# Kernel tuning notes

Measured on AMD Instinct MI355X. Metric: run time of the kernel, lower is better.

## Reference

```python
import jax, jax.numpy as jnp
import numpy as np

EPS = 1e-5      # BatchNorm eps
QLEV = 255.0    # 8-bit PACT activation levels (unsigned)
WMAX = 127.0    # int8 symmetric weight range


def _ste(x, q):
    # straight-through estimator: forward value q, gradient of x
    return x + jax.lax.stop_gradient(q - x)


def _wquant(w):
    # channel-wise symmetric int8 fake-quant of conv weights (per out-channel)
    s = jnp.maximum(jnp.max(jnp.abs(w), axis=(1, 2, 3), keepdims=True) / WMAX, 1e-8)
    q = jnp.clip(jnp.round(w / s), -WMAX, WMAX) * s
    return _ste(w, q)


def _conv3x3(x, w, stride=1):
    return jax.lax.conv_general_dilated(
        x, w, window_strides=(stride, stride), padding=((1, 1), (1, 1)),
        dimension_numbers=("NCHW", "OIHW", "NCHW"))


def _bn(x, g, b, m, v):
    # folded BatchNorm: per-channel affine with running stats
    return (x - m) * (g * jax.lax.rsqrt(v + EPS)) + b


def _pact(x, alpha):
    # PACT: clip to [0, alpha] then 8-bit per-channel fake-quant
    c = jnp.clip(x, 0.0, alpha)
    s = alpha / QLEV
    q = jnp.round(c / s) * s
    return _ste(c, q)


def _requant(x, s):
    # requantize onto common grid s (shift-based align in the int model)
    return _ste(x, jnp.round(x / s) * s)


def setup_inputs() -> dict:
    key = jax.random.key(0)
    ks = jax.random.split(key, 10)
    N, C, H, W = 32, 128, 56, 56
    x = jax.random.normal(ks[0], (N, C, H, W), jnp.float32)
    w1 = jax.random.normal(ks[1], (C, C, 3, 3), jnp.float32) * 0.05
    w2 = jax.random.normal(ks[2], (C, C, 3, 3), jnp.float32) * 0.05
    pc = (1, C, 1, 1)
    g1 = jnp.ones(pc, jnp.float32); b1 = jnp.zeros(pc, jnp.float32)
    m1 = jax.random.normal(ks[3], pc, jnp.float32) * 0.1
    v1 = jax.random.uniform(ks[4], pc, jnp.float32) + 0.5
    g2 = jnp.ones(pc, jnp.float32); b2 = jnp.zeros(pc, jnp.float32)
    m2 = jax.random.normal(ks[5], pc, jnp.float32) * 0.1
    v2 = jax.random.uniform(ks[6], pc, jnp.float32) + 0.5
    a1 = jax.random.uniform(ks[7], pc, jnp.float32) * 2.0 + 2.0
    a2 = jax.random.uniform(ks[8], pc, jnp.float32) * 2.0 + 2.0
    a3 = jax.random.uniform(ks[9], pc, jnp.float32) * 2.0 + 2.0
    return {"x": x, "w1": w1, "g1": g1, "b1": b1, "m1": m1, "v1": v1, "a1": a1,
            "w2": w2, "g2": g2, "b2": b2, "m2": m2, "v2": v2, "a2": a2, "a3": a3}


def reference(x, w1, g1, b1, m1, v1, a1, w2, g2, b2, m2, v2, a2, a3):
    # branch: quant-conv -> BN -> PACT-quant, twice
    out = _pact(_bn(_conv3x3(x, _wquant(w1)), g1, b1, m1, v1), a1)
    out = _pact(_bn(_conv3x3(out, _wquant(w2)), g2, b2, m2, v2), a2)
    # shift-based residual add: align both operands to act3's quant grid, add, clip+quant
    s3 = a3 / QLEV
    y = _requant(out, s3) + _requant(x, s3)
    return _pact(y, a3)
```

## Files before the change

kernel.cpp:

```cpp
#include <hip/hip_runtime.h>
#include <cstdint>

typedef __attribute__((ext_vector_type(4))) float f32x4;
typedef __attribute__((ext_vector_type(2))) float f32x2;
typedef __attribute__((ext_vector_type(4))) int int4v;
typedef __attribute__((ext_vector_type(4))) uint32_t uint4v;

#define EPSV 1e-5f

#define IMG   3136
#define NPIX  100352
#define PADTOT 13778944
#define S1Q (8.0f/127.0f)
#define S2Q (8.0f/(127.0f*254.0f))
#define S1A (4.0f/127.0f)
#define S2A (4.0f/(127.0f*254.0f))

#define UNPX 384
#define UNB  49152

__global__ __launch_bounds__(256) void k_prep(
    const float* __restrict__ x, const float* __restrict__ w1, const float* __restrict__ w2,
    const float* __restrict__ g1, const float* __restrict__ b1, const float* __restrict__ m1,
    const float* __restrict__ v1, const float* __restrict__ a1,
    const float* __restrict__ g2, const float* __restrict__ b2, const float* __restrict__ m2,
    const float* __restrict__ v2, const float* __restrict__ a2, const float* __restrict__ a3,
    int8_t* __restrict__ xq1, int8_t* __restrict__ xq2,
    int8_t* __restrict__ wj1, int8_t* __restrict__ wj2,
    char* __restrict__ o1k1, char* __restrict__ o1k2,
    f32x4* __restrict__ pp1, f32x4* __restrict__ pp2, f32x4* __restrict__ pp3,
    short* __restrict__ j3, int use_j3) {
  __shared__ float shf[7296];
  const int bid = blockIdx.x;
  const int t = threadIdx.x;

  if (bid < 1792) {
    int n = bid / 56, h = bid - (bid / 56) * 56;
    const float* base = x + (size_t)n * 401408 + h * 56;
    for (int idx = t; idx < 7168; idx += 256) {
      int ci = idx / 56, w = idx - (idx / 56) * 56;
      shf[ci * 57 + w] = base[ci * 3136 + w];
    }
    __syncthreads();
    const int ob = ((n * 58 + h + 1) * 58 + 1) * 128;
    for (int idx = t; idx < 1792; idx += 256) {
      int w = idx >> 5, c4 = (idx & 31) * 4;
      uint32_t p1 = 0, p2 = 0;
#pragma unroll
      for (int j = 0; j < 4; ++j) {
        float v = shf[(c4 + j) * 57 + w];
        float j1 = rintf(v * (127.0f / 8.0f));
        j1 = fminf(fmaxf(j1, -127.f), 127.f);
        float rr = v - j1 * S1Q;
        float j2 = rintf(rr * ((127.0f * 254.0f) / 8.0f));
        j2 = fminf(fmaxf(j2, -127.f), 127.f);
        p1 |= ((uint32_t)((int)j1 & 0xff)) << (8 * j);
        p2 |= ((uint32_t)((int)j2 & 0xff)) << (8 * j);
      }
      *(uint32_t*)(xq1 + ob + w * 128 + c4) = p1;
      *(uint32_t*)(xq2 + ob + w * 128 + c4) = p2;
    }
    if (use_j3) {
      const size_t jb = (size_t)n * 401408 + h * 56;
      for (int idx = t; idx < 7168; idx += 256) {
        int ci = idx / 56, w = idx - (idx / 56) * 56;
        float inv3 = 255.0f / a3[ci];
        j3[jb + ci * 3136 + w] = (short)(int)rintf(shf[ci * 57 + w] * inv3);
      }
    }
  } else if (bid < 1792 + 912) {
    int i = (bid - 1792) * 256 + t;
    int bi = i / 58368;
    int j = i - bi * 58368;
    char* buf = (bi == 0) ? (char*)xq1 : (bi == 1) ? (char*)xq2 : (bi == 2) ? o1k1 : o1k2;
    int n = j / 1824, cid = j - n * 1824;
    const int rowc = 58 * 8;
    int chunk;
    if (cid < rowc) chunk = cid;
    else if (cid < 2 * rowc) chunk = 57 * rowc + (cid - rowc);
    else {
      int e = cid - 2 * rowc;
      int h = 1 + (e >> 4);
      int r = e & 15;
      int w = (r < 8) ? 0 : 57;
      chunk = h * rowc + w * 8 + (r & 7);
    }
    long addr = ((long)n * 26912 + chunk) * 16;
    *(uint4v*)(buf + addr) = (uint4v){0u, 0u, 0u, 0u};
  } else {
    int sub = bid - 2704;
    int o = sub & 127;
    bool second = sub >= 128;
    const float* src = (second ? w2 : w1) + o * 1152;
    int8_t* wj = second ? wj2 : wj1;
    float* red = shf;
    float m = 0.f;
    for (int i = t; i < 1152; i += 256) m = fmaxf(m, fabsf(src[i]));
    red[t] = m;
    __syncthreads();
    for (int s = 128; s > 0; s >>= 1) {
      if (t < s) red[t] = fmaxf(red[t], red[t + s]);
      __syncthreads();
    }
    float s = fmaxf(red[0] / 127.0f, 1e-8f);
    for (int i = t; i < 1152; i += 256) {
      float q = rintf(src[i] / s);
      q = fminf(fmaxf(q, -127.f), 127.f);
      int ci = i / 9, tap = i - ci * 9;
      wj[(tap * 128 + o) * 128 + ci] = (int8_t)(int)q;
    }
    if (t == 0) {
      if (!second) {
        float r1 = 1.0f / sqrtf(v1[o] + EPSV);
        float sc1 = g1[o] * r1;
        pp1[o] = (f32x4){s * sc1, b1[o] - m1[o] * sc1, 255.0f / a1[o], a1[o] / 255.0f};
        pp3[o] = (f32x4){a3[o] / 255.0f, 255.0f / a3[o], a3[o], 0.0f};
      } else {
        float r2 = 1.0f / sqrtf(v2[o] + EPSV);
        float sc2 = g2[o] * r2;
        pp2[o] = (f32x4){s * sc2, b2[o] - m2[o] * sc2, 255.0f / a2[o], a2[o] / 255.0f};
      }
    }
  }
}


__global__ __launch_bounds__(512, 2) void k_conv1(
    const int8_t* __restrict__ xq1, const int8_t* __restrict__ xq2,
    const int8_t* __restrict__ wj1, const f32x4* __restrict__ pp1,
    int8_t* __restrict__ o1k1, int8_t* __restrict__ o1k2) {
  extern __shared__ char smem[];
  const int t = threadIdx.x;
  const int l = t & 63;
  const int wv = t >> 6;
  const int wr = wv >> 1;
  const int wc = wv & 1;
  const int lane15 = l & 15, hi4 = l >> 4;
  const int bid = blockIdx.x;
  const int px0 = ((bid & 7) * 98 + (bid >> 3)) * 128;

  unsigned n0 = (unsigned)px0 / IMG, r0 = (unsigned)px0 - n0 * IMG;
  unsigned h0 = r0 / 56, w0 = r0 - h0 * 56;
  const int base_idx = (int)((n0 * 58u + h0) * 58u + w0);
  const size_t base_byte = (size_t)base_idx * 128;

#pragma unroll
  for (int c = 0; c < 6; ++c) {
    const int pos = c * 512 + t;
    const int q = pos >> 3, s = pos & 7;
    const int lad = q * 128 + ((s ^ (q & 7)) * 16);
    *(int4v*)&smem[lad] = *(const int4v*)(xq1 + base_byte + (size_t)pos * 16);
    *(int4v*)&smem[UNB + lad] = *(const int4v*)(xq2 + base_byte + (size_t)pos * 16);
  }

  int u[4];
#pragma unroll
  for (int n2 = 0; n2 < 4; ++n2) {
    unsigned gpx = px0 + wc * 64 + n2 * 16 + lane15;
    unsigned n = gpx / IMG, rem = gpx - n * IMG, h = rem / 56, w = rem - h * 56;
    u[n2] = (int)((n * 58u + h) * 58u + w) - base_idx;
  }
  const int abase = (wr * 32 + lane15) * 128 + hi4 * 16;

  int4v acc1[2][4], acc2[2][4];
#pragma unroll
  for (int i = 0; i < 2; ++i)
#pragma unroll
    for (int j = 0; j < 4; ++j) { acc1[i][j] = (int4v){0,0,0,0}; acc2[i][j] = (int4v){0,0,0,0}; }

  __syncthreads();

#pragma unroll
  for (int tap = 0; tap < 9; ++tap) {
    const int td = (tap / 3) * 58 + (tap - (tap / 3) * 3);
    int4v a[2][2];
#pragma unroll
    for (int m = 0; m < 2; ++m)
#pragma unroll
      for (int kk = 0; kk < 2; ++kk)
        a[m][kk] = *(const int4v*)(wj1 + tap * 16384 + abase + m * 2048 + kk * 64);
#pragma unroll
    for (int kk = 0; kk < 2; ++kk) {
#pragma unroll
      for (int n2 = 0; n2 < 4; ++n2) {
        const int q = u[n2] + td;
        const int ad = q * 128 + (((kk * 4 + hi4) ^ (q & 7)) * 16);
        int4v bh = *(const int4v*)&smem[ad];
        int4v bl = *(const int4v*)&smem[UNB + ad];
        acc1[0][n2] = __builtin_amdgcn_mfma_i32_16x16x64_i8(a[0][kk], bh, acc1[0][n2], 0, 0, 0);
        acc1[1][n2] = __builtin_amdgcn_mfma_i32_16x16x64_i8(a[1][kk], bh, acc1[1][n2], 0, 0, 0);
        acc2[0][n2] = __builtin_amdgcn_mfma_i32_16x16x64_i8(a[0][kk], bl, acc2[0][n2], 0, 0, 0);
        acc2[1][n2] = __builtin_amdgcn_mfma_i32_16x16x64_i8(a[1][kk], bl, acc2[1][n2], 0, 0, 0);
      }
    }
  }

  __syncthreads();
  char* sT1 = smem;
  char* sT2 = smem + UNB;
#pragma unroll
  for (int m = 0; m < 2; ++m) {
    const int cobase = wr * 32 + m * 16 + 4 * hi4;
    const int slot = cobase >> 4, off = cobase & 15;
#pragma unroll
    for (int n2 = 0; n2 < 4; ++n2) {
      const int pxl = wc * 64 + n2 * 16 + lane15;
      uint32_t pk1 = 0, pk2 = 0;
#pragma unroll
      for (int r = 0; r < 4; ++r) {
        f32x4 p = pp1[cobase + r];
        float accf = (float)acc1[m][n2][r] * S1Q + (float)acc2[m][n2][r] * S2Q;
        float y = accf * p[0] + p[1];
        float cv = fminf(fmaxf(y, 0.f), p[3] * 255.0f);
        float act = rintf(cv * p[2]) * p[3];
        float k1 = fminf(rintf(act * (127.0f / 4.0f)), 127.f);
        float rr = act - k1 * S1A;
        float k2 = fminf(fmaxf(rintf(rr * ((127.0f * 254.0f) / 4.0f)), -127.f), 127.f);
        pk1 |= ((uint32_t)((int)k1 & 0xff)) << (8 * r);
        pk2 |= ((uint32_t)((int)k2 & 0xff)) << (8 * r);
      }
      const int ad = pxl * 128 + ((slot ^ (pxl & 7)) * 16) + off;
      *(uint32_t*)&sT1[ad] = pk1;
      *(uint32_t*)&sT2[ad] = pk2;
    }
  }
  __syncthreads();
  {
    const int pxl = t >> 2, q = t & 3;
    unsigned gpx = px0 + pxl;
    unsigned n = gpx / IMG;
    unsigned rem = gpx - n * IMG;
    unsigned h = rem / 56;
    unsigned w = rem - h * 56;
    int ob = (int)(((n * 58u + h + 1u) * 58u + (w + 1u)) * 128u);
#pragma unroll
    for (int i = 0; i < 2; ++i) {
      const int slot = q * 2 + i;
      const int ad = pxl * 128 + ((slot ^ (pxl & 7)) * 16);
      *(uint4v*)(o1k1 + ob + slot * 16) = *(uint4v*)&sT1[ad];
      *(uint4v*)(o1k2 + ob + slot * 16) = *(uint4v*)&sT2[ad];
    }
  }
}

__global__ __launch_bounds__(512, 2) void k_conv2(
    const int8_t* __restrict__ o1k1, const int8_t* __restrict__ o1k2,
    const int8_t* __restrict__ wj2, const f32x4* __restrict__ pp2,
    const f32x4* __restrict__ pp3, const float* __restrict__ x,
    const short* __restrict__ j3, int use_j3,
    float* __restrict__ out) {
  extern __shared__ char smem[];
  const int t = threadIdx.x;
  const int l = t & 63;
  const int wv = t >> 6;
  const int wr = wv >> 1, wc = wv & 1;
  const int lane15 = l & 15, hi4 = l >> 4;
  const int bid = blockIdx.x;
  const int px0 = ((bid & 7) * 98 + (bid >> 3)) * 128;

  unsigned n0 = (unsigned)px0 / IMG, r0 = (unsigned)px0 - n0 * IMG;
  unsigned h0 = r0 / 56, w0 = r0 - h0 * 56;
  const int base_idx = (int)((n0 * 58u + h0) * 58u + w0);
  const size_t base_byte = (size_t)base_idx * 128;

#pragma unroll
  for (int c = 0; c < 6; ++c) {
    const int pos = c * 512 + t;
    const int q = pos >> 3, s = pos & 7;
    const int lad = q * 128 + ((s ^ (q & 7)) * 16);
    *(int4v*)&smem[lad] = *(const int4v*)(o1k1 + base_byte + (size_t)pos * 16);
    *(int4v*)&smem[UNB + lad] = *(const int4v*)(o1k2 + base_byte + (size_t)pos * 16);
  }

  int u[4];
#pragma unroll
  for (int n2 = 0; n2 < 4; ++n2) {
    unsigned gpx = px0 + wc * 64 + n2 * 16 + lane15;
    unsigned n = gpx / IMG, rem = gpx - n * IMG, h = rem / 56, w = rem - h * 56;
    u[n2] = (int)((n * 58u + h) * 58u + w) - base_idx;
  }
  const int abase = (wr * 32 + lane15) * 128 + hi4 * 16;

  int4v acc1[2][4], acc2[2][4];
#pragma unroll
  for (int i = 0; i < 2; ++i)
#pragma unroll
    for (int j = 0; j < 4; ++j) { acc1[i][j] = (int4v){0,0,0,0}; acc2[i][j] = (int4v){0,0,0,0}; }

  __syncthreads();

#pragma unroll
  for (int tap = 0; tap < 9; ++tap) {
    const int td = (tap / 3) * 58 + (tap - (tap / 3) * 3);
    int4v a[2][2];
#pragma unroll
    for (int m = 0; m < 2; ++m)
#pragma unroll
      for (int kk = 0; kk < 2; ++kk)
        a[m][kk] = *(const int4v*)(wj2 + tap * 16384 + abase + m * 2048 + kk * 64);
#pragma unroll
    for (int kk = 0; kk < 2; ++kk) {
#pragma unroll
      for (int n2 = 0; n2 < 4; ++n2) {
        const int q = u[n2] + td;
        const int ad = q * 128 + (((kk * 4 + hi4) ^ (q & 7)) * 16);
        int4v bh = *(const int4v*)&smem[ad];
        int4v bl = *(const int4v*)&smem[UNB + ad];
        acc1[0][n2] = __builtin_amdgcn_mfma_i32_16x16x64_i8(a[0][kk], bh, acc1[0][n2], 0, 0, 0);
        acc1[1][n2] = __builtin_amdgcn_mfma_i32_16x16x64_i8(a[1][kk], bh, acc1[1][n2], 0, 0, 0);
        acc2[0][n2] = __builtin_amdgcn_mfma_i32_16x16x64_i8(a[0][kk], bl, acc2[0][n2], 0, 0, 0);
        acc2[1][n2] = __builtin_amdgcn_mfma_i32_16x16x64_i8(a[1][kk], bl, acc2[1][n2], 0, 0, 0);
      }
    }
  }

  float* E = (float*)smem;
  const int ppx = (t & 63) * 2;
  unsigned gpx0 = px0 + ppx;
  unsigned nn = gpx0 / IMG;
  unsigned rrem = gpx0 - nn * IMG;
  const size_t obase = (size_t)nn * 401408 + rrem;
  const int rowgrp = t >> 6;

  __syncthreads();
#pragma unroll
  for (int m = 0; m < 2; ++m) {
#pragma unroll
    for (int n2 = 0; n2 < 4; ++n2) {
      const int pxl = wc * 64 + n2 * 16 + lane15;
#pragma unroll
      for (int r = 0; r < 4; ++r) {
        const int co_l = wr * 16 + 4 * hi4 + r;
        E[co_l * 132 + pxl] = (float)acc1[m][n2][r] * S1A + (float)acc2[m][n2][r] * S2A;
      }
    }
    __syncthreads();
#pragma unroll
    for (int j = 0; j < 8; ++j) {
      const int co_l = j * 8 + rowgrp;
      const int co = (co_l >> 4) * 32 + m * 16 + (co_l & 15);
      const f32x4 p2 = pp2[co];
      const f32x4 p3 = pp3[co];
      const size_t off = obase + (size_t)co * 3136;
      float v0 = E[co_l * 132 + ppx];
      float v1 = E[co_l * 132 + ppx + 1];
      float rx0, rx1;
      if (use_j3) {
        const short* jp = j3 + off;
        rx0 = (float)jp[0] * p3[0];
        rx1 = (float)jp[1] * p3[0];
      } else {
        const float* xp = x + off;
        rx0 = rintf(xp[0] * p3[1]) * p3[0];
        rx1 = rintf(xp[1] * p3[1]) * p3[0];
      }
      float o0, o1;
      {
        float y = v0 * p2[0] + p2[1];
        float cv = fminf(fmaxf(y, 0.f), p2[3] * 255.0f);
        float act = rintf(cv * p2[2]) * p2[3];
        float ro = rintf(act * p3[1]) * p3[0];
        float y3 = ro + rx0;
        float c3 = fminf(fmaxf(y3, 0.f), p3[2]);
        o0 = rintf(c3 * p3[1]) * p3[0];
      }
      {
        float y = v1 * p2[0] + p2[1];
        float cv = fminf(fmaxf(y, 0.f), p2[3] * 255.0f);
        float act = rintf(cv * p2[2]) * p2[3];
        float ro = rintf(act * p3[1]) * p3[0];
        float y3 = ro + rx1;
        float c3 = fminf(fmaxf(y3, 0.f), p3[2]);
        o1 = rintf(c3 * p3[1]) * p3[0];
      }
      *(f32x2*)(out + off) = (f32x2){o0, o1};
    }
    __syncthreads();
  }
}

extern "C" void kernel_launch(void* const* d_in, const int* in_sizes, int n_in,
                              void* d_out, int out_size, void* d_ws, size_t ws_size,
                              hipStream_t stream) {
  (void)in_sizes; (void)n_in; (void)out_size;
  const float* x  = (const float*)d_in[0];
  const float* w1 = (const float*)d_in[1];
  const float* g1 = (const float*)d_in[2];
  const float* b1 = (const float*)d_in[3];
  const float* m1 = (const float*)d_in[4];
  const float* v1 = (const float*)d_in[5];
  const float* a1 = (const float*)d_in[6];
  const float* w2 = (const float*)d_in[7];
  const float* g2 = (const float*)d_in[8];
  const float* b2 = (const float*)d_in[9];
  const float* m2 = (const float*)d_in[10];
  const float* v2 = (const float*)d_in[11];
  const float* a2 = (const float*)d_in[12];
  const float* a3 = (const float*)d_in[13];

  char* ws = (char*)d_ws;
  int8_t* xq1  = (int8_t*)ws;
  int8_t* xq2  = (int8_t*)(ws + (size_t)PADTOT);
  int8_t* o1k1 = (int8_t*)(ws + 2 * (size_t)PADTOT);
  int8_t* o1k2 = (int8_t*)(ws + 3 * (size_t)PADTOT);
  int8_t* wj1  = (int8_t*)(ws + 4 * (size_t)PADTOT);
  int8_t* wj2  = (int8_t*)(ws + 4 * (size_t)PADTOT + 147456);
  f32x4*  pp1  = (f32x4*)(ws + 4 * (size_t)PADTOT + 2 * 147456);
  f32x4*  pp2  = pp1 + 128;
  f32x4*  pp3  = pp2 + 128;
  size_t j3off = 4 * (size_t)PADTOT + 2 * 147456 + 16384;
  short*  j3   = (short*)(ws + j3off);
  size_t need  = j3off + (size_t)NPIX * 128 * 2;
  int use_j3 = (ws_size >= need) ? 1 : 0;

  hipFuncSetAttribute((const void*)k_conv1, hipFuncAttributeMaxDynamicSharedMemorySize, 2 * UNB);
  hipFuncSetAttribute((const void*)k_conv2, hipFuncAttributeMaxDynamicSharedMemorySize, 2 * UNB);

  k_prep<<<2960, 256, 0, stream>>>(x, w1, w2, g1, b1, m1, v1, a1, g2, b2, m2, v2, a2, a3,
                                   xq1, xq2, wj1, wj2, (char*)o1k1, (char*)o1k2,
                                   pp1, pp2, pp3, j3, use_j3);
  k_conv1<<<784, 512, 2 * UNB, stream>>>(xq1, xq2, wj1, pp1, o1k1, o1k2);
  k_conv2<<<784, 512, 2 * UNB, stream>>>(o1k1, o1k2, wj2, pp2, pp3, x, j3, use_j3, (float*)d_out);
}
```

Measured before the change: 167.1 us.

## Split conv blocks over output-channel halves and stage input taps per iteration

Each conv block now computes 64 output channels for 128 pixels with 256 threads, where it used to compute 128 channels with 512 threads. Instead of preloading a 384-pixel halo window once, every tap loop reloads the shifted 128-pixel tile into a 32KB static LDS buffer. The aim is higher occupancy through smaller LDS use and more, smaller blocks, plus s_setprio around the MFMA section. The cost is that input tiles are re-read from global or L2 nine times per block and by both channel halves, with two barriers per tap.

```diff
diff --git a/kernel.cpp b/kernel.cpp
--- a/kernel.cpp
+++ b/kernel.cpp
@@ -15,9 +15,6 @@
 #define S2Q (8.0f/(127.0f*254.0f))
 #define S1A (4.0f/127.0f)
 #define S2A (4.0f/(127.0f*254.0f))
-
-#define UNPX 384
-#define UNB  49152
 
 __global__ __launch_bounds__(256) void k_prep(
     const float* __restrict__ x, const float* __restrict__ w1, const float* __restrict__ w2,
@@ -125,42 +122,38 @@
 }
 
 
-__global__ __launch_bounds__(512, 2) void k_conv1(
+__global__ __launch_bounds__(256, 4) void k_conv1(
     const int8_t* __restrict__ xq1, const int8_t* __restrict__ xq2,
     const int8_t* __restrict__ wj1, const f32x4* __restrict__ pp1,
     int8_t* __restrict__ o1k1, int8_t* __restrict__ o1k2) {
-  extern __shared__ char smem[];
+  __shared__ char smem[32768];
+  char* Bh = smem;
+  char* Bl = smem + 16384;
   const int t = threadIdx.x;
   const int l = t & 63;
   const int wv = t >> 6;
   const int wr = wv >> 1;
   const int wc = wv & 1;
   const int lane15 = l & 15, hi4 = l >> 4;
-  const int bid = blockIdx.x;
-  const int px0 = ((bid & 7) * 98 + (bid >> 3)) * 128;
-
-  unsigned n0 = (unsigned)px0 / IMG, r0 = (unsigned)px0 - n0 * IMG;
-  unsigned h0 = r0 / 56, w0 = r0 - h0 * 56;
-  const int base_idx = (int)((n0 * 58u + h0) * 58u + w0);
-  const size_t base_byte = (size_t)base_idx * 128;
-
-#pragma unroll
-  for (int c = 0; c < 6; ++c) {
-    const int pos = c * 512 + t;
-    const int q = pos >> 3, s = pos & 7;
-    const int lad = q * 128 + ((s ^ (q & 7)) * 16);
-    *(int4v*)&smem[lad] = *(const int4v*)(xq1 + base_byte + (size_t)pos * 16);
-    *(int4v*)&smem[UNB + lad] = *(const int4v*)(xq2 + base_byte + (size_t)pos * 16);
-  }
-
-  int u[4];
-#pragma unroll
-  for (int n2 = 0; n2 < 4; ++n2) {
-    unsigned gpx = px0 + wc * 64 + n2 * 16 + lane15;
-    unsigned n = gpx / IMG, rem = gpx - n * IMG, h = rem / 56, w = rem - h * 56;
-    u[n2] = (int)((n * 58u + h) * 58u + w) - base_idx;
-  }
-  const int abase = (wr * 32 + lane15) * 128 + hi4 * 16;
+  const int sw = ((blockIdx.x & 7) * 196) + (blockIdx.x >> 3);
+  const int cohalf = sw & 1;
+  const int px0 = (sw >> 1) * 128;
+  const int srow = t >> 1, sseg = t & 1;
+
+  int pixbyte;
+  {
+    unsigned gpx = px0 + srow;
+    unsigned n = gpx / IMG;
+    unsigned rem = gpx - n * IMG;
+    unsigned h = rem / 56;
+    unsigned w = rem - h * 56;
+    pixbyte = (int)(((n * 58u + h) * 58u + w) * 128u);
+  }
+  int lad[4];
+#pragma unroll
+  for (int j = 0; j < 4; ++j)
+    lad[j] = srow * 128 + (((sseg * 4 + j) ^ (srow & 7)) * 16);
+  const int abase = (cohalf * 64 + wr * 32 + lane15) * 128 + hi4 * 16;
 
   int4v acc1[2][4], acc2[2][4];
 #pragma unroll
@@ -168,47 +161,61 @@
 #pragma unroll
     for (int j = 0; j < 4; ++j) { acc1[i][j] = (int4v){0,0,0,0}; acc2[i][j] = (int4v){0,0,0,0}; }
 
-  __syncthreads();
-
-#pragma unroll
+#pragma unroll 1
   for (int tap = 0; tap < 9; ++tap) {
-    const int td = (tap / 3) * 58 + (tap - (tap / 3) * 3);
+    const int kh = tap / 3, kw = tap - kh * 3;
+    const int toff = (kh * 58 + kw) * 128 + sseg * 64;
+    __syncthreads();
+    int4v s1[4], s2[4];
+#pragma unroll
+    for (int j = 0; j < 4; ++j) {
+      s1[j] = *(const int4v*)(xq1 + pixbyte + toff + j * 16);
+      s2[j] = *(const int4v*)(xq2 + pixbyte + toff + j * 16);
+    }
+#pragma unroll
+    for (int j = 0; j < 4; ++j) {
+      *(int4v*)&Bh[lad[j]] = s1[j];
+      *(int4v*)&Bl[lad[j]] = s2[j];
+    }
+    __syncthreads();
+    __builtin_amdgcn_s_setprio(1);
     int4v a[2][2];
 #pragma unroll
-    for (int m = 0; m < 2; ++m)
-#pragma unroll
-      for (int kk = 0; kk < 2; ++kk)
-        a[m][kk] = *(const int4v*)(wj1 + tap * 16384 + abase + m * 2048 + kk * 64);
+    for (int kk = 0; kk < 2; ++kk)
+#pragma unroll
+      for (int m = 0; m < 2; ++m)
+        a[kk][m] = *(const int4v*)(wj1 + tap * 16384 + abase + m * 2048 + kk * 64);
 #pragma unroll
     for (int kk = 0; kk < 2; ++kk) {
 #pragma unroll
       for (int n2 = 0; n2 < 4; ++n2) {
-        const int q = u[n2] + td;
-        const int ad = q * 128 + (((kk * 4 + hi4) ^ (q & 7)) * 16);
-        int4v bh = *(const int4v*)&smem[ad];
-        int4v bl = *(const int4v*)&smem[UNB + ad];
-        acc1[0][n2] = __builtin_amdgcn_mfma_i32_16x16x64_i8(a[0][kk], bh, acc1[0][n2], 0, 0, 0);
-        acc1[1][n2] = __builtin_amdgcn_mfma_i32_16x16x64_i8(a[1][kk], bh, acc1[1][n2], 0, 0, 0);
-        acc2[0][n2] = __builtin_amdgcn_mfma_i32_16x16x64_i8(a[0][kk], bl, acc2[0][n2], 0, 0, 0);
-        acc2[1][n2] = __builtin_amdgcn_mfma_i32_16x16x64_i8(a[1][kk], bl, acc2[1][n2], 0, 0, 0);
-      }
-    }
+        const int row = wc * 64 + n2 * 16 + lane15;
+        const int ad = row * 128 + (((kk * 4 + hi4) ^ (row & 7)) * 16);
+        int4v bh = *(const int4v*)&Bh[ad];
+        int4v bl = *(const int4v*)&Bl[ad];
+        acc1[0][n2] = __builtin_amdgcn_mfma_i32_16x16x64_i8(a[kk][0], bh, acc1[0][n2], 0, 0, 0);
+        acc1[1][n2] = __builtin_amdgcn_mfma_i32_16x16x64_i8(a[kk][1], bh, acc1[1][n2], 0, 0, 0);
+        acc2[0][n2] = __builtin_amdgcn_mfma_i32_16x16x64_i8(a[kk][0], bl, acc2[0][n2], 0, 0, 0);
+        acc2[1][n2] = __builtin_amdgcn_mfma_i32_16x16x64_i8(a[kk][1], bl, acc2[1][n2], 0, 0, 0);
+      }
+    }
+    __builtin_amdgcn_s_setprio(0);
   }
 
   __syncthreads();
   char* sT1 = smem;
-  char* sT2 = smem + UNB;
+  char* sT2 = smem + 16384;
 #pragma unroll
   for (int m = 0; m < 2; ++m) {
-    const int cobase = wr * 32 + m * 16 + 4 * hi4;
-    const int slot = cobase >> 4, off = cobase & 15;
+    const int cob = wr * 32 + m * 16 + 4 * hi4;
+    const int slot = cob >> 4, off = cob & 15;
 #pragma unroll
     for (int n2 = 0; n2 < 4; ++n2) {
       const int pxl = wc * 64 + n2 * 16 + lane15;
       uint32_t pk1 = 0, pk2 = 0;
 #pragma unroll
       for (int r = 0; r < 4; ++r) {
-        f32x4 p = pp1[cobase + r];
+        f32x4 p = pp1[cohalf * 64 + cob + r];
         float accf = (float)acc1[m][n2][r] * S1Q + (float)acc2[m][n2][r] * S2Q;
         float y = accf * p[0] + p[1];
         float cv = fminf(fmaxf(y, 0.f), p[3] * 255.0f);
@@ -219,67 +226,63 @@
         pk1 |= ((uint32_t)((int)k1 & 0xff)) << (8 * r);
         pk2 |= ((uint32_t)((int)k2 & 0xff)) << (8 * r);
       }
-      const int ad = pxl * 128 + ((slot ^ (pxl & 7)) * 16) + off;
+      const int ad = pxl * 64 + ((slot ^ (pxl & 3)) * 16) + off;
       *(uint32_t*)&sT1[ad] = pk1;
       *(uint32_t*)&sT2[ad] = pk2;
     }
   }
   __syncthreads();
   {
-    const int pxl = t >> 2, q = t & 3;
+    const int pxl = t >> 1, seg = t & 1;
     unsigned gpx = px0 + pxl;
     unsigned n = gpx / IMG;
     unsigned rem = gpx - n * IMG;
     unsigned h = rem / 56;
     unsigned w = rem - h * 56;
-    int ob = (int)(((n * 58u + h + 1u) * 58u + (w + 1u)) * 128u);
+    int ob = (int)(((n * 58u + h + 1u) * 58u + (w + 1u)) * 128u) + cohalf * 64;
 #pragma unroll
     for (int i = 0; i < 2; ++i) {
-      const int slot = q * 2 + i;
-      const int ad = pxl * 128 + ((slot ^ (pxl & 7)) * 16);
+      const int slot = seg * 2 + i;
+      const int ad = pxl * 64 + ((slot ^ (pxl & 3)) * 16);
       *(uint4v*)(o1k1 + ob + slot * 16) = *(uint4v*)&sT1[ad];
       *(uint4v*)(o1k2 + ob + slot * 16) = *(uint4v*)&sT2[ad];
     }
   }
 }
 
-__global__ __launch_bounds__(512, 2) void k_conv2(
+__global__ __launch_bounds__(256, 4) void k_conv2(
     const int8_t* __restrict__ o1k1, const int8_t* __restrict__ o1k2,
     const int8_t* __restrict__ wj2, const f32x4* __restrict__ pp2,
     const f32x4* __restrict__ pp3, const float* __restrict__ x,
     const short* __restrict__ j3, int use_j3,
     float* __restrict__ out) {
-  extern __shared__ char smem[];
+  __shared__ char smem[32768];
+  char* Bh = smem;
+  char* Bl = smem + 16384;
   const int t = threadIdx.x;
   const int l = t & 63;
   const int wv = t >> 6;
   const int wr = wv >> 1, wc = wv & 1;
   const int lane15 = l & 15, hi4 = l >> 4;
-  const int bid = blockIdx.x;
-  const int px0 = ((bid & 7) * 98 + (bid >> 3)) * 128;
-
-  unsigned n0 = (unsigned)px0 / IMG, r0 = (unsigned)px0 - n0 * IMG;
-  unsigned h0 = r0 / 56, w0 = r0 - h0 * 56;
-  const int base_idx = (int)((n0 * 58u + h0) * 58u + w0);
-  const size_t base_byte = (size_t)base_idx * 128;
-
-#pragma unroll
-  for (int c = 0; c < 6; ++c) {
-    const int pos = c * 512 + t;
-    const int q = pos >> 3, s = pos & 7;
-    const int lad = q * 128 + ((s ^ (q & 7)) * 16);
-    *(int4v*)&smem[lad] = *(const int4v*)(o1k1 + base_byte + (size_t)pos * 16);
-    *(int4v*)&smem[UNB + lad] = *(const int4v*)(o1k2 + base_byte + (size_t)pos * 16);
-  }
-
-  int u[4];
-#pragma unroll
-  for (int n2 = 0; n2 < 4; ++n2) {
-    unsigned gpx = px0 + wc * 64 + n2 * 16 + lane15;
-    unsigned n = gpx / IMG, rem = gpx - n * IMG, h = rem / 56, w = rem - h * 56;
-    u[n2] = (int)((n * 58u + h) * 58u + w) - base_idx;
-  }
-  const int abase = (wr * 32 + lane15) * 128 + hi4 * 16;
+  const int sw = ((blockIdx.x & 7) * 196) + (blockIdx.x >> 3);
+  const int cohalf = sw & 1;
+  const int px0 = (sw >> 1) * 128;
+  const int srow = t >> 1, sseg = t & 1;
+
+  int pixbyte;
+  {
+    unsigned gpx = px0 + srow;
+    unsigned n = gpx / IMG;
+    unsigned rem = gpx - n * IMG;
+    unsigned h = rem / 56;
+    unsigned w = rem - h * 56;
+    pixbyte = (int)(((n * 58u + h) * 58u + w) * 128u);
+  }
+  int lad[4];
+#pragma unroll
+  for (int j = 0; j < 4; ++j)
+    lad[j] = srow * 128 + (((sseg * 4 + j) ^ (srow & 7)) * 16);
+  const int abase = (cohalf * 64 + wr * 32 + lane15) * 128 + hi4 * 16;
 
   int4v acc1[2][4], acc2[2][4];
 #pragma unroll
@@ -287,40 +290,54 @@
 #pragma unroll
     for (int j = 0; j < 4; ++j) { acc1[i][j] = (int4v){0,0,0,0}; acc2[i][j] = (int4v){0,0,0,0}; }
 
-  __syncthreads();
-
-#pragma unroll
+#pragma unroll 1
   for (int tap = 0; tap < 9; ++tap) {
-    const int td = (tap / 3) * 58 + (tap - (tap / 3) * 3);
+    const int kh = tap / 3, kw = tap - kh * 3;
+    const int toff = (kh * 58 + kw) * 128 + sseg * 64;
+    __syncthreads();
+    int4v s1[4], s2[4];
+#pragma unroll
+    for (int j = 0; j < 4; ++j) {
+      s1[j] = *(const int4v*)(o1k1 + pixbyte + toff + j * 16);
+      s2[j] = *(const int4v*)(o1k2 + pixbyte + toff + j * 16);
+    }
+#pragma unroll
+    for (int j = 0; j < 4; ++j) {
+      *(int4v*)&Bh[lad[j]] = s1[j];
+      *(int4v*)&Bl[lad[j]] = s2[j];
+    }
+    __syncthreads();
+    __builtin_amdgcn_s_setprio(1);
     int4v a[2][2];
 #pragma unroll
-    for (int m = 0; m < 2; ++m)
-#pragma unroll
-      for (int kk = 0; kk < 2; ++kk)
-        a[m][kk] = *(const int4v*)(wj2 + tap * 16384 + abase + m * 2048 + kk * 64);
+    for (int kk = 0; kk < 2; ++kk)
+#pragma unroll
+      for (int m = 0; m < 2; ++m)
+        a[kk][m] = *(const int4v*)(wj2 + tap * 16384 + abase + m * 2048 + kk * 64);
 #pragma unroll
     for (int kk = 0; kk < 2; ++kk) {
 #pragma unroll
       for (int n2 = 0; n2 < 4; ++n2) {
-        const int q = u[n2] + td;
-        const int ad = q * 128 + (((kk * 4 + hi4) ^ (q & 7)) * 16);
-        int4v bh = *(const int4v*)&smem[ad];
-        int4v bl = *(const int4v*)&smem[UNB + ad];
-        acc1[0][n2] = __builtin_amdgcn_mfma_i32_16x16x64_i8(a[0][kk], bh, acc1[0][n2], 0, 0, 0);
-        acc1[1][n2] = __builtin_amdgcn_mfma_i32_16x16x64_i8(a[1][kk], bh, acc1[1][n2], 0, 0, 0);
-        acc2[0][n2] = __builtin_amdgcn_mfma_i32_16x16x64_i8(a[0][kk], bl, acc2[0][n2], 0, 0, 0);
-        acc2[1][n2] = __builtin_amdgcn_mfma_i32_16x16x64_i8(a[1][kk], bl, acc2[1][n2], 0, 0, 0);
-      }
-    }
+        const int row = wc * 64 + n2 * 16 + lane15;
+        const int ad = row * 128 + (((kk * 4 + hi4) ^ (row & 7)) * 16);
+        int4v bh = *(const int4v*)&Bh[ad];
+        int4v bl = *(const int4v*)&Bl[ad];
+        acc1[0][n2] = __builtin_amdgcn_mfma_i32_16x16x64_i8(a[kk][0], bh, acc1[0][n2], 0, 0, 0);
+        acc1[1][n2] = __builtin_amdgcn_mfma_i32_16x16x64_i8(a[kk][1], bh, acc1[1][n2], 0, 0, 0);
+        acc2[0][n2] = __builtin_amdgcn_mfma_i32_16x16x64_i8(a[kk][0], bl, acc2[0][n2], 0, 0, 0);
+        acc2[1][n2] = __builtin_amdgcn_mfma_i32_16x16x64_i8(a[kk][1], bl, acc2[1][n2], 0, 0, 0);
+      }
+    }
+    __builtin_amdgcn_s_setprio(0);
   }
 
   float* E = (float*)smem;
-  const int ppx = (t & 63) * 2;
-  unsigned gpx0 = px0 + ppx;
+  const int co_g = t >> 6;
+  const int px2 = (t & 63) * 2;
+  unsigned gpx0 = px0 + px2;
   unsigned nn = gpx0 / IMG;
   unsigned rrem = gpx0 - nn * IMG;
   const size_t obase = (size_t)nn * 401408 + rrem;
-  const int rowgrp = t >> 6;
 
   __syncthreads();
 #pragma unroll
@@ -337,13 +354,13 @@
     __syncthreads();
 #pragma unroll
     for (int j = 0; j < 8; ++j) {
-      const int co_l = j * 8 + rowgrp;
-      const int co = (co_l >> 4) * 32 + m * 16 + (co_l & 15);
+      const int co_l = j * 4 + co_g;
+      const int co = cohalf * 64 + (co_l >> 4) * 32 + m * 16 + (co_l & 15);
       const f32x4 p2 = pp2[co];
       const f32x4 p3 = pp3[co];
       const size_t off = obase + (size_t)co * 3136;
-      float v0 = E[co_l * 132 + ppx];
-      float v1 = E[co_l * 132 + ppx + 1];
+      float v0 = E[co_l * 132 + px2];
+      float v1 = E[co_l * 132 + px2 + 1];
       float rx0, rx1;
       if (use_j3) {
         const short* jp = j3 + off;
@@ -413,12 +430,9 @@
   size_t need  = j3off + (size_t)NPIX * 128 * 2;
   int use_j3 = (ws_size >= need) ? 1 : 0;
 
-  hipFuncSetAttribute((const void*)k_conv1, hipFuncAttributeMaxDynamicSharedMemorySize, 2 * UNB);
-  hipFuncSetAttribute((const void*)k_conv2, hipFuncAttributeMaxDynamicSharedMemorySize, 2 * UNB);
-
   k_prep<<<2960, 256, 0, stream>>>(x, w1, w2, g1, b1, m1, v1, a1, g2, b2, m2, v2, a2, a3,
                                    xq1, xq2, wj1, wj2, (char*)o1k1, (char*)o1k2,
                                    pp1, pp2, pp3, j3, use_j3);
-  k_conv1<<<784, 512, 2 * UNB, stream>>>(xq1, xq2, wj1, pp1, o1k1, o1k2);
-  k_conv2<<<784, 512, 2 * UNB, stream>>>(o1k1, o1k2, wj2, pp2, pp3, x, j3, use_j3, (float*)d_out);
+  k_conv1<<<1568, 256, 0, stream>>>(xq1, xq2, wj1, pp1, o1k1, o1k2);
+  k_conv2<<<1568, 256, 0, stream>>>(o1k1, o1k2, wj2, pp2, pp3, x, j3, use_j3, (float*)d_out);
 }
```

After: 183.5 us. 1.1x slower.
